# Optimization experiments

Hardware: AMD Instinct MI355X
Metric: run time of the kernel (lower is better)

## Reference

```python
import jax, jax.numpy as jnp
import numpy as np
import math

E, K, CAPF = 8, 2, 1.25
D, DFF = 512, 2048


def setup_inputs() -> dict:
    key = jax.random.key(0)
    ks = jax.random.split(key, 5)
    s = lambda k, sh, sc: (jax.random.normal(k, sh, jnp.float32) * sc)
    return {
        "x": jax.random.normal(ks[0], (8, 4096, D), jnp.float32),
        "Wr": s(ks[1], (D, E), 1.0 / math.sqrt(D)),
        "br": jnp.zeros((E,), jnp.float32),
        "W1": s(ks[2], (E, D, DFF), 1.0 / math.sqrt(D)),
        "b1": jnp.zeros((E, DFF), jnp.float32),
        "W2": s(ks[3], (E, DFF, D), 1.0 / math.sqrt(DFF)),
        "b2": jnp.zeros((E, D), jnp.float32),
    }


def _moe(x, Wr, br, W1, b1, W2, b2):
    orig = x.shape
    d = orig[-1]
    xf = x.reshape(-1, d)                     # [N, d]
    N = xf.shape[0]
    # --- TopK router ---
    logits = xf @ Wr + br                      # [N, E]
    probs = jax.nn.softmax(logits, axis=-1)
    topk_p, topk_i = jax.lax.top_k(probs, K)   # [N, K]
    topk_w = topk_p / (jnp.sum(topk_p, axis=-1, keepdims=True) + 1e-9)
    # --- Capacity-based sparse dispatch ---
    cap = max(1, int(math.ceil(CAPF * float(N * K) / float(E))))
    flat_e = topk_i.reshape(-1)                # [N*K] expert id per slot
    flat_w = topk_w.reshape(-1)                # [N*K]
    tok = jnp.repeat(jnp.arange(N), K)         # [N*K] source token id
    one_hot = jax.nn.one_hot(flat_e, E, dtype=xf.dtype)          # [N*K, E]
    pos = (jnp.cumsum(one_hot, axis=0) - one_hot)[jnp.arange(N * K), flat_e]
    pos = pos.astype(jnp.int32)                # position within expert buffer
    keep = pos < cap                           # tokens beyond capacity dropped
    w_k = jnp.where(keep, flat_w, 0.0)
    sum_w = jnp.zeros((N,), xf.dtype).at[tok].add(w_k)           # kept weight per token
    w_norm = w_k / (sum_w[tok] + 1e-9)
    slot = flat_e * cap + pos                  # flat index into [E*cap]
    slot_safe = jnp.where(keep, slot, E * cap) # out-of-bounds -> dropped by scatter
    expert_in = (jnp.zeros((E * cap, d), xf.dtype)
                 .at[slot_safe].set(xf[tok], mode="drop")
                 .reshape(E, cap, d))
    # --- Grouped expert FFN (exact GELU like torch nn.GELU) ---
    h = jax.nn.gelu(jnp.einsum("ecd,edf->ecf", expert_in, W1) + b1[:, None, :],
                    approximate=False)
    expert_out = (jnp.einsum("ecf,efd->ecd", h, W2) + b2[:, None, :]).reshape(E * cap, d)
    # --- Combine: gather back and weighted scatter-add per token ---
    contrib = expert_out[jnp.where(keep, slot, 0)]               # dropped -> w_norm=0
    y = jnp.zeros((N, d), xf.dtype).at[tok].add(contrib * w_norm[:, None])
    return y.reshape(orig)


def reference(x, Wr, br, W1, b1, W2, b2):
    return _moe(x, Wr, br, W1, b1, W2, b2)
```

## Files before the change

kernel.cpp:

```cpp
#include <hip/hip_runtime.h>
#include <cstdint>
#include <cstddef>

#define E_EXP 8
#define TOPK 2
#define DMODEL 512
#define DFFDIM 2048

typedef __attribute__((ext_vector_type(8))) short short8;
typedef __attribute__((ext_vector_type(4))) float f32x4;

__device__ __forceinline__ unsigned short f2bf(float f) {
    unsigned int u = __float_as_uint(f);
    u += 0x7fffu + ((u >> 16) & 1u);
    return (unsigned short)(u >> 16);
}

__device__ __forceinline__ void gld_lds16(const unsigned short* g, unsigned short* l) {
    __builtin_amdgcn_global_load_lds(
        (const __attribute__((address_space(1))) void*)g,
        (__attribute__((address_space(3))) void*)l, 16, 0, 0);
}

__global__ __launch_bounds__(256) void transpose_kernel(
    const float* __restrict__ in, unsigned short* __restrict__ out, int R, int C)
{
    __shared__ float tile[32][33];
    const float* ie = in + (size_t)blockIdx.z * R * C;
    unsigned short* oe = out + (size_t)blockIdx.z * R * C;
    int x = blockIdx.x * 32 + threadIdx.x;
#pragma unroll
    for (int i = 0; i < 4; i++) {
        int ry = blockIdx.y * 32 + threadIdx.y + i * 8;
        tile[threadIdx.y + i * 8][threadIdx.x] = ie[(size_t)ry * C + x];
    }
    __syncthreads();
    int xo = blockIdx.y * 32 + threadIdx.x;
#pragma unroll
    for (int i = 0; i < 4; i++) {
        int co = blockIdx.x * 32 + threadIdx.y + i * 8;
        oe[(size_t)co * R + xo] = f2bf(tile[threadIdx.x][threadIdx.y + i * 8]);
    }
}

__global__ __launch_bounds__(256) void router_kernel(
    const float* __restrict__ x, const float* __restrict__ Wr,
    const float* __restrict__ br, int N,
    int* __restrict__ e0e1, float2* __restrict__ w01)
{
    int lane = threadIdx.x & 63, wave = threadIdx.x >> 6;
    int t = blockIdx.x * 4 + wave;
    if (t >= N) return;
    const float* xr = x + (size_t)t * DMODEL;
    float4 v0 = *(const float4*)(xr + lane * 4);
    float4 v1 = *(const float4*)(xr + 256 + lane * 4);
    float xv[8] = {v0.x, v0.y, v0.z, v0.w, v1.x, v1.y, v1.z, v1.w};
    const float* wr0 = Wr + (size_t)lane * 32;
    const float* wr1 = Wr + (size_t)(256 + lane * 4) * 8;
    double acc[8];
#pragma unroll
    for (int j = 0; j < 8; j++) acc[j] = 0.0;
#pragma unroll
    for (int c = 0; c < 4; c++) {
#pragma unroll
        for (int j = 0; j < 8; j++) {
            acc[j] += (double)xv[c] * (double)wr0[c * 8 + j];
            acc[j] += (double)xv[4 + c] * (double)wr1[c * 8 + j];
        }
    }
#pragma unroll
    for (int j = 0; j < 8; j++) {
        double s = acc[j];
#pragma unroll
        for (int o = 32; o > 0; o >>= 1) s += __shfl_xor(s, o, 64);
        acc[j] = s;
    }
    if (lane == 0) {
        float l[8], p[8];
        float mx = -1e30f;
        for (int j = 0; j < 8; j++) { l[j] = (float)acc[j] + br[j]; mx = fmaxf(mx, l[j]); }
        float Z = 0.f;
        for (int j = 0; j < 8; j++) { p[j] = expf(l[j] - mx); Z += p[j]; }
        for (int j = 0; j < 8; j++) p[j] /= Z;
        int e0 = 0;
        for (int j = 1; j < 8; j++) if (l[j] > l[e0]) e0 = j;
        int e1 = (e0 == 0) ? 1 : 0;
        for (int j = 0; j < 8; j++) if (j != e0 && l[j] > l[e1]) e1 = j;
        float den = p[e0] + p[e1] + 1e-9f;
        e0e1[t] = e0 | (e1 << 8);
        w01[t] = make_float2(p[e0] / den, p[e1] / den);
    }
}

__global__ __launch_bounds__(256) void hist_kernel(
    const int* __restrict__ e0e1, int NK, int* __restrict__ hist)
{
    __shared__ int cnt[8];
    int t = threadIdx.x;
    if (t < 8) cnt[t] = 0;
    __syncthreads();
    int s = blockIdx.x * 256 + t;
    if (s < NK) {
        int pk = e0e1[s >> 1];
        int e = (s & 1) ? ((pk >> 8) & 255) : (pk & 255);
        atomicAdd(&cnt[e], 1);
    }
    __syncthreads();
    if (t < 8) hist[blockIdx.x * 8 + t] = cnt[t];
}

__global__ __launch_bounds__(256) void scan_kernel(
    const int* __restrict__ hist, int NB, int cap,
    int* __restrict__ base, int* __restrict__ cnt_used)
{
    __shared__ int buf[256];
    int t = threadIdx.x;
    for (int e = 0; e < 8; e++) {
        int v = (t < NB) ? hist[t * 8 + e] : 0;
        int val = v;
        buf[t] = val;
        __syncthreads();
        for (int o = 1; o < 256; o <<= 1) {
            int add = (t >= o) ? buf[t - o] : 0;
            __syncthreads();
            val += add;
            buf[t] = val;
            __syncthreads();
        }
        if (t < NB) base[t * 8 + e] = val - v;
        if (t == 255) cnt_used[e] = min(val, cap);
        __syncthreads();
    }
}

__global__ __launch_bounds__(256) void pos_kernel(
    const int* __restrict__ e0e1, const float2* __restrict__ w01,
    const int* __restrict__ base, int NK, int cap,
    int* __restrict__ sidx, int* __restrict__ tok_of, float* __restrict__ wslot)
{
    __shared__ int waveCnt[4][8];
    __shared__ float kw[256];
    int t = threadIdx.x, lane = t & 63, wave = t >> 6;
    int s = blockIdx.x * 256 + t;
    bool valid = s < NK;
    int e = 8; float w = 0.f;
    if (valid) {
        int pk = e0e1[s >> 1];
        float2 ww = w01[s >> 1];
        if (s & 1) { e = (pk >> 8) & 255; w = ww.y; }
        else       { e = pk & 255;        w = ww.x; }
    }
    unsigned long long mymask = 0ull;
#pragma unroll
    for (int j = 0; j < 8; j++) {
        unsigned long long m = __ballot(e == j);
        if (lane == j) waveCnt[wave][j] = __popcll(m);
        if (e == j) mymask = m;
    }
    __syncthreads();
    int wrank = __popcll(mymask & ((1ull << lane) - 1ull));
    int prior = 0;
    for (int w2 = 0; w2 < wave; w2++) prior += waveCnt[w2][e & 7];
    int pos = base[blockIdx.x * 8 + (e & 7)] + prior + wrank;
    bool keep = valid && (pos < cap);
    kw[t] = keep ? w : 0.f;
    __syncthreads();
    float sum = kw[t] + kw[t ^ 1];
    float wn = keep ? (kw[t] / (sum + 1e-9f)) : 0.f;
    if (valid) {
        int si = keep ? (e * cap + pos) : -1;
        sidx[s] = si;
        if (keep) { tok_of[si] = s >> 1; wslot[si] = wn; }
    }
}

__global__ __launch_bounds__(256) void scatter_kernel(
    const float* __restrict__ x, const int* __restrict__ sidx,
    unsigned short* __restrict__ Xe, int NK)
{
    int lane = threadIdx.x & 63, wave = threadIdx.x >> 6;
    int s = blockIdx.x * 4 + wave;
    if (s >= NK) return;
    int si = sidx[s];
    if (si < 0) return;
    int tok = s >> 1;
    const float* xr = x + (size_t)tok * DMODEL + lane * 8;
    float4 a = *(const float4*)xr;
    float4 b = *(const float4*)(xr + 4);
    short8 v;
    v[0] = (short)f2bf(a.x); v[1] = (short)f2bf(a.y);
    v[2] = (short)f2bf(a.z); v[3] = (short)f2bf(a.w);
    v[4] = (short)f2bf(b.x); v[5] = (short)f2bf(b.y);
    v[6] = (short)f2bf(b.z); v[7] = (short)f2bf(b.w);
    *(short8*)(Xe + (size_t)si * DMODEL + lane * 8) = v;
}

template <int MODE>
__global__ __launch_bounds__(256, 3) void gemm_kernel(
    const unsigned short* __restrict__ A, int lda, size_t aStrE,
    const unsigned short* __restrict__ B, int ldb, size_t bStrE,
    const float* __restrict__ bias, int biasStrE,
    void* __restrict__ out, size_t cStrE, int ldc,
    const int* __restrict__ cnt, const int* __restrict__ tok_of,
    const float* __restrict__ wslot, int cap, int Kext)
{
    __shared__ unsigned short As[2 * 128 * 32];
    __shared__ unsigned short Bs[2 * 128 * 32];
    int e = blockIdx.z;
    int m0 = blockIdx.y * 128, n0 = blockIdx.x * 128;
    int M = cnt[e];
    if (m0 >= M) return;
    const unsigned short* Ae = A + (size_t)e * aStrE;
    const unsigned short* Be = B + (size_t)e * bStrE;

    int t = threadIdx.x, lane = t & 63, wave = t >> 6;
    int row = t >> 2;
    int seg = ((t & 3) ^ ((t >> 3) & 3)) * 8;
    const unsigned short* ga = Ae + (size_t)(m0 + row) * lda + seg;
    const unsigned short* gb = Be + (size_t)(n0 + row) * ldb + seg;
    int wofs = __builtin_amdgcn_readfirstlane(wave * 512);

    f32x4 acc[4][4];
#pragma unroll
    for (int i = 0; i < 4; i++)
#pragma unroll
        for (int j = 0; j < 4; j++) acc[i][j] = (f32x4){0.f, 0.f, 0.f, 0.f};

    int wm = (wave & 1) * 64, wn = (wave >> 1) * 64;
    int lr = lane & 15, lq = lane >> 4;
    int sq = (lq ^ ((lr >> 1) & 3)) * 8;
    const unsigned short* pa = As + (wm + lr) * 32 + sq;
    const unsigned short* pb = Bs + (wn + lr) * 32 + sq;

    gld_lds16(ga, As + wofs);
    gld_lds16(ga + (size_t)64 * lda, As + 2048 + wofs);
    gld_lds16(gb, Bs + wofs);
    gld_lds16(gb + (size_t)64 * ldb, Bs + 2048 + wofs);
    ga += 32; gb += 32;
    __syncthreads();

    int buf = 0;
    for (int k0 = 32; k0 < Kext; k0 += 32) {
        int nbo = (buf ^ 1) * 4096;
        gld_lds16(ga, As + nbo + wofs);
        gld_lds16(ga + (size_t)64 * lda, As + nbo + 2048 + wofs);
        gld_lds16(gb, Bs + nbo + wofs);
        gld_lds16(gb + (size_t)64 * ldb, Bs + nbo + 2048 + wofs);
        ga += 32; gb += 32;
        {
            int bo = buf * 4096;
            short8 af[4], bfv[4];
#pragma unroll
            for (int i = 0; i < 4; i++) af[i] = *(const short8*)(pa + bo + i * 512);
#pragma unroll
            for (int j = 0; j < 4; j++) bfv[j] = *(const short8*)(pb + bo + j * 512);
#pragma unroll
            for (int i = 0; i < 4; i++)
#pragma unroll
                for (int j = 0; j < 4; j++)
                    acc[i][j] = __builtin_amdgcn_mfma_f32_16x16x32_bf16(af[i], bfv[j], acc[i][j], 0, 0, 0);
        }
        __syncthreads();
        buf ^= 1;
    }
    {
        int bo = buf * 4096;
        short8 af[4], bfv[4];
#pragma unroll
        for (int i = 0; i < 4; i++) af[i] = *(const short8*)(pa + bo + i * 512);
#pragma unroll
        for (int j = 0; j < 4; j++) bfv[j] = *(const short8*)(pb + bo + j * 512);
#pragma unroll
        for (int i = 0; i < 4; i++)
#pragma unroll
            for (int j = 0; j < 4; j++)
                acc[i][j] = __builtin_amdgcn_mfma_f32_16x16x32_bf16(af[i], bfv[j], acc[i][j], 0, 0, 0);
    }

    if (MODE == 0) {
        size_t cb = (size_t)e * cStrE;
#pragma unroll
        for (int j = 0; j < 4; j++) {
            int n = n0 + wn + j * 16 + lr;
            float bv = bias[(size_t)e * biasStrE + n];
#pragma unroll
            for (int i = 0; i < 4; i++) {
                int mbase = m0 + wm + i * 16 + lq * 4;
                f32x4 v = acc[i][j];
#pragma unroll
                for (int r = 0; r < 4; r++) {
                    float val = v[r] + bv;
                    val = 0.5f * val * (1.0f + erff(val * 0.7071067811865475f));
                    ((unsigned short*)out)[cb + (size_t)(mbase + r) * ldc + n] = f2bf(val);
                }
            }
        }
    } else {
        float wv[4][4]; int tv[4][4];
#pragma unroll
        for (int i = 0; i < 4; i++) {
            int mbase = m0 + wm + i * 16 + lq * 4;
#pragma unroll
            for (int r = 0; r < 4; r++) {
                int m = mbase + r;
                if (m < M) { int sl = e * cap + m; wv[i][r] = wslot[sl]; tv[i][r] = tok_of[sl]; }
                else       { wv[i][r] = 0.f; tv[i][r] = -1; }
            }
        }
        float* y = (float*)out;
#pragma unroll
        for (int j = 0; j < 4; j++) {
            int n = n0 + wn + j * 16 + lr;
            float bv = bias[(size_t)e * biasStrE + n];
#pragma unroll
            for (int i = 0; i < 4; i++) {
                f32x4 v = acc[i][j];
#pragma unroll
                for (int r = 0; r < 4; r++) {
                    if (tv[i][r] >= 0)
                        atomicAdd(y + (size_t)tv[i][r] * ldc + n, wv[i][r] * (v[r] + bv));
                }
            }
        }
    }
}

extern "C" void kernel_launch(void* const* d_in, const int* in_sizes, int n_in,
                              void* d_out, int out_size, void* d_ws, size_t ws_size,
                              hipStream_t stream)
{
    const float* x  = (const float*)d_in[0];
    const float* Wr = (const float*)d_in[1];
    const float* br = (const float*)d_in[2];
    const float* W1 = (const float*)d_in[3];
    const float* b1 = (const float*)d_in[4];
    const float* W2 = (const float*)d_in[5];
    const float* b2 = (const float*)d_in[6];
    float* y = (float*)d_out;
    (void)n_in;

    const int N = in_sizes[0] / DMODEL;
    const int NK = N * TOPK;
    const int cap = (NK * 5 + 31) / 32;
    const int mTiles = (cap + 127) / 128;
    const int NB = (NK + 255) / 256;

    size_t fixed = (size_t)E_EXP * DMODEL * DFFDIM * 2 * 2
                 + (size_t)E_EXP * cap * DMODEL * 2
                 + (size_t)N * 12 + (size_t)NK * 4 + (size_t)E_EXP * cap * 8
                 + (size_t)NB * 64 + (1 << 16);
    int G = E_EXP;
    while (G > 1 && fixed + (size_t)G * cap * DFFDIM * 2 > ws_size) G >>= 1;
    const int nGroups = E_EXP / G;

    char* ws = (char*)d_ws;
    size_t off = 0;
    auto take = [&](size_t bytes) {
        char* p = ws + off;
        off = (off + bytes + 255) & ~(size_t)255;
        return p;
    };
    unsigned short* W1t = (unsigned short*)take((size_t)E_EXP * DMODEL * DFFDIM * 2);
    unsigned short* W2t = (unsigned short*)take((size_t)E_EXP * DMODEL * DFFDIM * 2);
    unsigned short* Xe  = (unsigned short*)take((size_t)E_EXP * cap * DMODEL * 2);
    unsigned short* Hg  = (unsigned short*)take((size_t)G * cap * DFFDIM * 2);
    int*    e0e1 = (int*)take((size_t)N * 4);
    float2* w01  = (float2*)take((size_t)N * 8);
    int*    hist = (int*)take((size_t)NB * 8 * 4);
    int*    base = (int*)take((size_t)NB * 8 * 4);
    int*    cnt  = (int*)take(64);
    int*    sidx = (int*)take((size_t)NK * 4);
    int*    tok_of = (int*)take((size_t)E_EXP * cap * 4);
    float*  wslot  = (float*)take((size_t)E_EXP * cap * 4);

    transpose_kernel<<<dim3(DFFDIM / 32, DMODEL / 32, E_EXP), dim3(32, 8), 0, stream>>>(W1, W1t, DMODEL, DFFDIM);
    transpose_kernel<<<dim3(DMODEL / 32, DFFDIM / 32, E_EXP), dim3(32, 8), 0, stream>>>(W2, W2t, DFFDIM, DMODEL);
    router_kernel<<<(N + 3) / 4, 256, 0, stream>>>(x, Wr, br, N, e0e1, w01);
    hist_kernel<<<NB, 256, 0, stream>>>(e0e1, NK, hist);
    scan_kernel<<<1, 256, 0, stream>>>(hist, NB, cap, base, cnt);
    pos_kernel<<<NB, 256, 0, stream>>>(e0e1, w01, base, NK, cap, sidx, tok_of, wslot);
    scatter_kernel<<<(NK + 3) / 4, 256, 0, stream>>>(x, sidx, Xe, NK);
    hipMemsetAsync(d_out, 0, (size_t)out_size * 4, stream);

    for (int g = 0; g < nGroups; g++) {
        int e0 = g * G;
        gemm_kernel<0><<<dim3(DFFDIM / 128, mTiles, G), 256, 0, stream>>>(
            Xe + (size_t)e0 * cap * DMODEL, DMODEL, (size_t)cap * DMODEL,
            W1t + (size_t)e0 * DFFDIM * DMODEL, DMODEL, (size_t)DFFDIM * DMODEL,
            b1 + (size_t)e0 * DFFDIM, DFFDIM,
            Hg, (size_t)cap * DFFDIM, DFFDIM,
            cnt + e0, tok_of, wslot, cap, DMODEL);
        gemm_kernel<1><<<dim3(DMODEL / 128, mTiles, G), 256, 0, stream>>>(
            Hg, DFFDIM, (size_t)cap * DFFDIM,
            W2t + (size_t)e0 * DMODEL * DFFDIM, DFFDIM, (size_t)DMODEL * DFFDIM,
            b2 + (size_t)e0 * DMODEL, DMODEL,
            y, 0, DMODEL,
            cnt + e0, tok_of + (size_t)e0 * cap, wslot + (size_t)e0 * cap, cap, DFFDIM);
    }
}
```

Measured before the change: 993.6 us.

## Use 256x256 GEMM tiles and split DFF into four quarter passes

The expert GEMMs move from 128x128 tiles with 256 threads to 256x256 tiles with 512 threads, K-step 64, and a wider LDS swizzle. Larger tiles give more reuse per loaded byte. The FFN hidden dimension is now processed in four quarter-DFF passes over all experts. Each pass writes a smaller H buffer, and the second GEMM accumulates partial sums into y with atomics, adding bias only on the first pass. This trades a fixed, smaller workspace for four times as many atomic output updates and fewer blocks per launch, which risks tail and occupancy losses.

```diff
diff --git a/kernel.cpp b/kernel.cpp
--- a/kernel.cpp
+++ b/kernel.cpp
@@ -196,82 +196,104 @@
 }
 
 template <int MODE>
-__global__ __launch_bounds__(256, 3) void gemm_kernel(
+__global__ __launch_bounds__(512, 2) void gemm256_kernel(
     const unsigned short* __restrict__ A, int lda, size_t aStrE,
     const unsigned short* __restrict__ B, int ldb, size_t bStrE,
     const float* __restrict__ bias, int biasStrE,
     void* __restrict__ out, size_t cStrE, int ldc,
     const int* __restrict__ cnt, const int* __restrict__ tok_of,
-    const float* __restrict__ wslot, int cap, int Kext)
-{
-    __shared__ unsigned short As[2 * 128 * 32];
-    __shared__ unsigned short Bs[2 * 128 * 32];
+    const float* __restrict__ wslot, int cap, int Kext, int addBias)
+{
+    __shared__ unsigned short As[2 * 16384];
+    __shared__ unsigned short Bs[2 * 16384];
     int e = blockIdx.z;
-    int m0 = blockIdx.y * 128, n0 = blockIdx.x * 128;
+    int m0 = blockIdx.y * 256, n0 = blockIdx.x * 256;
     int M = cnt[e];
     if (m0 >= M) return;
     const unsigned short* Ae = A + (size_t)e * aStrE;
     const unsigned short* Be = B + (size_t)e * bStrE;
 
     int t = threadIdx.x, lane = t & 63, wave = t >> 6;
-    int row = t >> 2;
-    int seg = ((t & 3) ^ ((t >> 3) & 3)) * 8;
-    const unsigned short* ga = Ae + (size_t)(m0 + row) * lda + seg;
-    const unsigned short* gb = Be + (size_t)(n0 + row) * ldb + seg;
+    int srow = t >> 3;
+    int gseg = ((t & 7) ^ (srow & 7)) * 8;
+    const unsigned short* ga = Ae + (size_t)(m0 + srow) * lda + gseg;
+    const unsigned short* gb = Be + (size_t)(n0 + srow) * ldb + gseg;
     int wofs = __builtin_amdgcn_readfirstlane(wave * 512);
 
-    f32x4 acc[4][4];
-#pragma unroll
-    for (int i = 0; i < 4; i++)
+    f32x4 acc[8][4];
+#pragma unroll
+    for (int i = 0; i < 8; i++)
 #pragma unroll
         for (int j = 0; j < 4; j++) acc[i][j] = (f32x4){0.f, 0.f, 0.f, 0.f};
 
-    int wm = (wave & 1) * 64, wn = (wave >> 1) * 64;
+    int wm = (wave >> 2) * 128, wn = (wave & 3) * 64;
     int lr = lane & 15, lq = lane >> 4;
-    int sq = (lq ^ ((lr >> 1) & 3)) * 8;
-    const unsigned short* pa = As + (wm + lr) * 32 + sq;
-    const unsigned short* pb = Bs + (wn + lr) * 32 + sq;
-
-    gld_lds16(ga, As + wofs);
-    gld_lds16(ga + (size_t)64 * lda, As + 2048 + wofs);
-    gld_lds16(gb, Bs + wofs);
-    gld_lds16(gb + (size_t)64 * ldb, Bs + 2048 + wofs);
-    ga += 32; gb += 32;
+    int s0 = ((lq) ^ (lr & 7)) * 8;
+    int s1 = ((lq + 4) ^ (lr & 7)) * 8;
+    const unsigned short* pa = As + (wm + lr) * 64;
+    const unsigned short* pb = Bs + (wn + lr) * 64;
+
+    const int nt = Kext >> 6;
+
+#pragma unroll
+    for (int u = 0; u < 4; u++) {
+        gld_lds16(ga + (size_t)(u * 64) * lda, As + u * 4096 + wofs);
+        gld_lds16(gb + (size_t)(u * 64) * ldb, Bs + u * 4096 + wofs);
+    }
     __syncthreads();
 
     int buf = 0;
-    for (int k0 = 32; k0 < Kext; k0 += 32) {
-        int nbo = (buf ^ 1) * 4096;
-        gld_lds16(ga, As + nbo + wofs);
-        gld_lds16(ga + (size_t)64 * lda, As + nbo + 2048 + wofs);
-        gld_lds16(gb, Bs + nbo + wofs);
-        gld_lds16(gb + (size_t)64 * ldb, Bs + nbo + 2048 + wofs);
-        ga += 32; gb += 32;
+    for (int ks = 1; ks < nt; ks++) {
+        int nbo = (buf ^ 1) * 16384;
+        int k0 = ks * 64;
+#pragma unroll
+        for (int u = 0; u < 4; u++) {
+            gld_lds16(ga + (size_t)(u * 64) * lda + k0, As + nbo + u * 4096 + wofs);
+            gld_lds16(gb + (size_t)(u * 64) * ldb + k0, Bs + nbo + u * 4096 + wofs);
+        }
         {
-            int bo = buf * 4096;
-            short8 af[4], bfv[4];
-#pragma unroll
-            for (int i = 0; i < 4; i++) af[i] = *(const short8*)(pa + bo + i * 512);
-#pragma unroll
-            for (int j = 0; j < 4; j++) bfv[j] = *(const short8*)(pb + bo + j * 512);
-#pragma unroll
-            for (int i = 0; i < 4; i++)
+            int bo = buf * 16384;
+            short8 af[8], bfv[4];
+#pragma unroll
+            for (int i = 0; i < 8; i++) af[i] = *(const short8*)(pa + bo + i * 1024 + s0);
+#pragma unroll
+            for (int j = 0; j < 4; j++) bfv[j] = *(const short8*)(pb + bo + j * 1024 + s0);
+#pragma unroll
+            for (int i = 0; i < 8; i++)
 #pragma unroll
                 for (int j = 0; j < 4; j++)
                     acc[i][j] = __builtin_amdgcn_mfma_f32_16x16x32_bf16(af[i], bfv[j], acc[i][j], 0, 0, 0);
+#pragma unroll
+            for (int i = 0; i < 8; i++) af[i] = *(const short8*)(pa + bo + i * 1024 + s1);
+#pragma unroll
+            for (int j = 0; j < 4; j++) bfv[j] = *(const short8*)(pb + bo + j * 1024 + s1);
+#pragma unroll
+            for (int i = 0; i < 8; i++)
+#pragma unroll
+                for (int j = 0; j < 4; j++)
+                    acc[i][j] = __builtin_amdgcn_mfma_f32_16x16x32_bf16(af[i], bfv[j], acc[i][j], 0, 0, 0);
         }
         __syncthreads();
         buf ^= 1;
     }
     {
-        int bo = buf * 4096;
-        short8 af[4], bfv[4];
-#pragma unroll
-        for (int i = 0; i < 4; i++) af[i] = *(const short8*)(pa + bo + i * 512);
-#pragma unroll
-        for (int j = 0; j < 4; j++) bfv[j] = *(const short8*)(pb + bo + j * 512);
-#pragma unroll
-        for (int i = 0; i < 4; i++)
+        int bo = buf * 16384;
+        short8 af[8], bfv[4];
+#pragma unroll
+        for (int i = 0; i < 8; i++) af[i] = *(const short8*)(pa + bo + i * 1024 + s0);
+#pragma unroll
+        for (int j = 0; j < 4; j++) bfv[j] = *(const short8*)(pb + bo + j * 1024 + s0);
+#pragma unroll
+        for (int i = 0; i < 8; i++)
+#pragma unroll
+            for (int j = 0; j < 4; j++)
+                acc[i][j] = __builtin_amdgcn_mfma_f32_16x16x32_bf16(af[i], bfv[j], acc[i][j], 0, 0, 0);
+#pragma unroll
+        for (int i = 0; i < 8; i++) af[i] = *(const short8*)(pa + bo + i * 1024 + s1);
+#pragma unroll
+        for (int j = 0; j < 4; j++) bfv[j] = *(const short8*)(pb + bo + j * 1024 + s1);
+#pragma unroll
+        for (int i = 0; i < 8; i++)
 #pragma unroll
             for (int j = 0; j < 4; j++)
                 acc[i][j] = __builtin_amdgcn_mfma_f32_16x16x32_bf16(af[i], bfv[j], acc[i][j], 0, 0, 0);
@@ -284,7 +306,7 @@
             int n = n0 + wn + j * 16 + lr;
             float bv = bias[(size_t)e * biasStrE + n];
 #pragma unroll
-            for (int i = 0; i < 4; i++) {
+            for (int i = 0; i < 8; i++) {
                 int mbase = m0 + wm + i * 16 + lq * 4;
                 f32x4 v = acc[i][j];
 #pragma unroll
@@ -296,9 +318,9 @@
             }
         }
     } else {
-        float wv[4][4]; int tv[4][4];
-#pragma unroll
-        for (int i = 0; i < 4; i++) {
+        float wv[8][4]; int tv[8][4];
+#pragma unroll
+        for (int i = 0; i < 8; i++) {
             int mbase = m0 + wm + i * 16 + lq * 4;
 #pragma unroll
             for (int r = 0; r < 4; r++) {
@@ -311,9 +333,9 @@
 #pragma unroll
         for (int j = 0; j < 4; j++) {
             int n = n0 + wn + j * 16 + lr;
-            float bv = bias[(size_t)e * biasStrE + n];
-#pragma unroll
-            for (int i = 0; i < 4; i++) {
+            float bv = addBias ? bias[(size_t)e * biasStrE + n] : 0.f;
+#pragma unroll
+            for (int i = 0; i < 8; i++) {
                 f32x4 v = acc[i][j];
 #pragma unroll
                 for (int r = 0; r < 4; r++) {
@@ -337,21 +359,14 @@
     const float* W2 = (const float*)d_in[5];
     const float* b2 = (const float*)d_in[6];
     float* y = (float*)d_out;
-    (void)n_in;
+    (void)n_in; (void)ws_size;
 
     const int N = in_sizes[0] / DMODEL;
     const int NK = N * TOPK;
     const int cap = (NK * 5 + 31) / 32;
-    const int mTiles = (cap + 127) / 128;
+    const int mT = (cap + 255) / 256;
     const int NB = (NK + 255) / 256;
-
-    size_t fixed = (size_t)E_EXP * DMODEL * DFFDIM * 2 * 2
-                 + (size_t)E_EXP * cap * DMODEL * 2
-                 + (size_t)N * 12 + (size_t)NK * 4 + (size_t)E_EXP * cap * 8
-                 + (size_t)NB * 64 + (1 << 16);
-    int G = E_EXP;
-    while (G > 1 && fixed + (size_t)G * cap * DFFDIM * 2 > ws_size) G >>= 1;
-    const int nGroups = E_EXP / G;
+    const int QD = DFFDIM / 4;
 
     char* ws = (char*)d_ws;
     size_t off = 0;
@@ -363,7 +378,7 @@
     unsigned short* W1t = (unsigned short*)take((size_t)E_EXP * DMODEL * DFFDIM * 2);
     unsigned short* W2t = (unsigned short*)take((size_t)E_EXP * DMODEL * DFFDIM * 2);
     unsigned short* Xe  = (unsigned short*)take((size_t)E_EXP * cap * DMODEL * 2);
-    unsigned short* Hg  = (unsigned short*)take((size_t)G * cap * DFFDIM * 2);
+    unsigned short* Hg  = (unsigned short*)take((size_t)E_EXP * cap * QD * 2);
     int*    e0e1 = (int*)take((size_t)N * 4);
     float2* w01  = (float2*)take((size_t)N * 8);
     int*    hist = (int*)take((size_t)NB * 8 * 4);
@@ -382,19 +397,18 @@
     scatter_kernel<<<(NK + 3) / 4, 256, 0, stream>>>(x, sidx, Xe, NK);
     hipMemsetAsync(d_out, 0, (size_t)out_size * 4, stream);
 
-    for (int g = 0; g < nGroups; g++) {
-        int e0 = g * G;
-        gemm_kernel<0><<<dim3(DFFDIM / 128, mTiles, G), 256, 0, stream>>>(
-            Xe + (size_t)e0 * cap * DMODEL, DMODEL, (size_t)cap * DMODEL,
-            W1t + (size_t)e0 * DFFDIM * DMODEL, DMODEL, (size_t)DFFDIM * DMODEL,
-            b1 + (size_t)e0 * DFFDIM, DFFDIM,
-            Hg, (size_t)cap * DFFDIM, DFFDIM,
-            cnt + e0, tok_of, wslot, cap, DMODEL);
-        gemm_kernel<1><<<dim3(DMODEL / 128, mTiles, G), 256, 0, stream>>>(
-            Hg, DFFDIM, (size_t)cap * DFFDIM,
-            W2t + (size_t)e0 * DMODEL * DFFDIM, DFFDIM, (size_t)DMODEL * DFFDIM,
-            b2 + (size_t)e0 * DMODEL, DMODEL,
+    for (int q = 0; q < 4; q++) {
+        gemm256_kernel<0><<<dim3(QD / 256, mT, E_EXP), 512, 0, stream>>>(
+            Xe, DMODEL, (size_t)cap * DMODEL,
+            W1t + (size_t)q * QD * DMODEL, DMODEL, (size_t)DFFDIM * DMODEL,
+            b1 + q * QD, DFFDIM,
+            Hg, (size_t)cap * QD, QD,
+            cnt, tok_of, wslot, cap, DMODEL, 1);
+        gemm256_kernel<1><<<dim3(DMODEL / 256, mT, E_EXP), 512, 0, stream>>>(
+            Hg, QD, (size_t)cap * QD,
+            W2t + (size_t)q * QD, DFFDIM, (size_t)DMODEL * DFFDIM,
+            b2, DMODEL,
             y, 0, DMODEL,
-            cnt + e0, tok_of + (size_t)e0 * cap, wslot + (size_t)e0 * cap, cap, DFFDIM);
-    }
-}
+            cnt, tok_of, wslot, cap, QD, q == 0 ? 1 : 0);
+    }
+}
```

Measured after the change: 1.468 ms. +47.8%, slower.

## Fuse expert FFN GEMMs with gather into one persistent per-tile kernel

Applied to the files above, without the earlier changes.

Replaces the scatter kernel and the two grouped GEMM launches with a single kernel. Each block gathers its 128 routed token rows straight from x, converting them to bf16 in registers. It then streams W1 and W2 in 32-column DFF chunks, applies GELU on chip and accumulates the output projection in registers before the atomic combine. This removes the bf16 Xe buffer and the large H intermediate round trip through memory, along with several launches. In exchange, each block rereads its expert's full weights. Register pressure is high (a 128-float accumulator per lane plus the cached A fragments), and the tile count assumes cap is a multiple of 128.

```diff
diff --git a/kernel.cpp b/kernel.cpp
--- a/kernel.cpp
+++ b/kernel.cpp
@@ -136,7 +136,7 @@
 __global__ __launch_bounds__(256) void pos_kernel(
     const int* __restrict__ e0e1, const float2* __restrict__ w01,
     const int* __restrict__ base, int NK, int cap,
-    int* __restrict__ sidx, int* __restrict__ tok_of, float* __restrict__ wslot)
+    int* __restrict__ tok_of, float* __restrict__ wslot)
 {
     __shared__ int waveCnt[4][8];
     __shared__ float kw[256];
@@ -167,160 +167,142 @@
     __syncthreads();
     float sum = kw[t] + kw[t ^ 1];
     float wn = keep ? (kw[t] / (sum + 1e-9f)) : 0.f;
-    if (valid) {
-        int si = keep ? (e * cap + pos) : -1;
-        sidx[s] = si;
-        if (keep) { tok_of[si] = s >> 1; wslot[si] = wn; }
-    }
-}
-
-__global__ __launch_bounds__(256) void scatter_kernel(
-    const float* __restrict__ x, const int* __restrict__ sidx,
-    unsigned short* __restrict__ Xe, int NK)
-{
-    int lane = threadIdx.x & 63, wave = threadIdx.x >> 6;
-    int s = blockIdx.x * 4 + wave;
-    if (s >= NK) return;
-    int si = sidx[s];
-    if (si < 0) return;
-    int tok = s >> 1;
-    const float* xr = x + (size_t)tok * DMODEL + lane * 8;
-    float4 a = *(const float4*)xr;
-    float4 b = *(const float4*)(xr + 4);
-    short8 v;
-    v[0] = (short)f2bf(a.x); v[1] = (short)f2bf(a.y);
-    v[2] = (short)f2bf(a.z); v[3] = (short)f2bf(a.w);
-    v[4] = (short)f2bf(b.x); v[5] = (short)f2bf(b.y);
-    v[6] = (short)f2bf(b.z); v[7] = (short)f2bf(b.w);
-    *(short8*)(Xe + (size_t)si * DMODEL + lane * 8) = v;
-}
-
-template <int MODE>
-__global__ __launch_bounds__(256, 3) void gemm_kernel(
-    const unsigned short* __restrict__ A, int lda, size_t aStrE,
-    const unsigned short* __restrict__ B, int ldb, size_t bStrE,
-    const float* __restrict__ bias, int biasStrE,
-    void* __restrict__ out, size_t cStrE, int ldc,
+    if (keep) {
+        int si = e * cap + pos;
+        tok_of[si] = s >> 1;
+        wslot[si] = wn;
+    }
+}
+
+__global__ __launch_bounds__(512, 2) void fused_ffn_kernel(
+    const float* __restrict__ x,
+    const unsigned short* __restrict__ W1t,
+    const float* __restrict__ b1,
+    const unsigned short* __restrict__ W2t,
+    const float* __restrict__ b2,
+    float* __restrict__ y,
     const int* __restrict__ cnt, const int* __restrict__ tok_of,
-    const float* __restrict__ wslot, int cap, int Kext)
-{
-    __shared__ unsigned short As[2 * 128 * 32];
-    __shared__ unsigned short Bs[2 * 128 * 32];
-    int e = blockIdx.z;
-    int m0 = blockIdx.y * 128, n0 = blockIdx.x * 128;
+    const float* __restrict__ wslot, int cap)
+{
+    __shared__ unsigned short Wb[2][32768];
+    __shared__ unsigned short Hlds[8 * 640];
+
+    int b = blockIdx.x;
+    int e = b & 7, mtile = b >> 3;
+    int m0 = mtile * 128;
     int M = cnt[e];
     if (m0 >= M) return;
-    const unsigned short* Ae = A + (size_t)e * aStrE;
-    const unsigned short* Be = B + (size_t)e * bStrE;
-
-    int t = threadIdx.x, lane = t & 63, wave = t >> 6;
-    int row = t >> 2;
-    int seg = ((t & 3) ^ ((t >> 3) & 3)) * 8;
-    const unsigned short* ga = Ae + (size_t)(m0 + row) * lda + seg;
-    const unsigned short* gb = Be + (size_t)(n0 + row) * ldb + seg;
-    int wofs = __builtin_amdgcn_readfirstlane(wave * 512);
-
-    f32x4 acc[4][4];
-#pragma unroll
-    for (int i = 0; i < 4; i++)
-#pragma unroll
-        for (int j = 0; j < 4; j++) acc[i][j] = (f32x4){0.f, 0.f, 0.f, 0.f};
-
-    int wm = (wave & 1) * 64, wn = (wave >> 1) * 64;
+
+    int t = threadIdx.x, lane = t & 63, w = t >> 6;
     int lr = lane & 15, lq = lane >> 4;
-    int sq = (lq ^ ((lr >> 1) & 3)) * 8;
-    const unsigned short* pa = As + (wm + lr) * 32 + sq;
-    const unsigned short* pb = Bs + (wn + lr) * 32 + sq;
-
-    gld_lds16(ga, As + wofs);
-    gld_lds16(ga + (size_t)64 * lda, As + 2048 + wofs);
-    gld_lds16(gb, Bs + wofs);
-    gld_lds16(gb + (size_t)64 * ldb, Bs + 2048 + wofs);
-    ga += 32; gb += 32;
+
+    const unsigned short* W1e = W1t + (size_t)e * DFFDIM * DMODEL;
+    const unsigned short* W2e = W2t + (size_t)e * DMODEL * DFFDIM;
+
+    int mrowA = m0 + w * 16 + lr;
+    int tokA = (mrowA < M) ? tok_of[e * cap + mrowA] : -1;
+    const float* xr = x + (size_t)(tokA < 0 ? 0 : tokA) * DMODEL;
+    short8 a_frag[16];
+#pragma unroll
+    for (int kf = 0; kf < 16; kf++) {
+        float4 u0 = *(const float4*)(xr + kf * 32 + lq * 8);
+        float4 u1 = *(const float4*)(xr + kf * 32 + lq * 8 + 4);
+        short8 f;
+        f[0] = (short)f2bf(u0.x); f[1] = (short)f2bf(u0.y);
+        f[2] = (short)f2bf(u0.z); f[3] = (short)f2bf(u0.w);
+        f[4] = (short)f2bf(u1.x); f[5] = (short)f2bf(u1.y);
+        f[6] = (short)f2bf(u1.z); f[7] = (short)f2bf(u1.w);
+        if (tokA < 0) f = (short8){0, 0, 0, 0, 0, 0, 0, 0};
+        a_frag[kf] = f;
+    }
+
+    f32x4 yac[32];
+#pragma unroll
+    for (int j = 0; j < 32; j++) yac[j] = (f32x4){0.f, 0.f, 0.f, 0.f};
+
+    unsigned short* Hl = Hlds + w * 640;
+    int l2 = lane >> 2;
+    int w2seg = (((lane & 3) ^ (l2 & 3)) * 8);
+    int w1seg = (lane ^ w) * 8;
+
+    {
+        int f0 = 0;
+#pragma unroll
+        for (int q = 0; q < 4; q++) {
+            int f = q * 8 + w;
+            gld_lds16(W1e + (size_t)(f0 + f) * DMODEL + w1seg,
+                      &Wb[0][q * 4096 + w * 512]);
+            int n = q * 128 + w * 16 + l2;
+            gld_lds16(W2e + (size_t)n * DFFDIM + f0 + w2seg,
+                      &Wb[0][16384 + q * 4096 + w * 512]);
+        }
+    }
     __syncthreads();
 
     int buf = 0;
-    for (int k0 = 32; k0 < Kext; k0 += 32) {
-        int nbo = (buf ^ 1) * 4096;
-        gld_lds16(ga, As + nbo + wofs);
-        gld_lds16(ga + (size_t)64 * lda, As + nbo + 2048 + wofs);
-        gld_lds16(gb, Bs + nbo + wofs);
-        gld_lds16(gb + (size_t)64 * ldb, Bs + nbo + 2048 + wofs);
-        ga += 32; gb += 32;
-        {
-            int bo = buf * 4096;
-            short8 af[4], bfv[4];
-#pragma unroll
-            for (int i = 0; i < 4; i++) af[i] = *(const short8*)(pa + bo + i * 512);
-#pragma unroll
-            for (int j = 0; j < 4; j++) bfv[j] = *(const short8*)(pb + bo + j * 512);
-#pragma unroll
-            for (int i = 0; i < 4; i++)
-#pragma unroll
-                for (int j = 0; j < 4; j++)
-                    acc[i][j] = __builtin_amdgcn_mfma_f32_16x16x32_bf16(af[i], bfv[j], acc[i][j], 0, 0, 0);
+    for (int c = 0; c < 64; c++) {
+        if (c < 63) {
+            int f0 = (c + 1) * 32;
+#pragma unroll
+            for (int q = 0; q < 4; q++) {
+                int f = q * 8 + w;
+                gld_lds16(W1e + (size_t)(f0 + f) * DMODEL + w1seg,
+                          &Wb[buf ^ 1][q * 4096 + w * 512]);
+                int n = q * 128 + w * 16 + l2;
+                gld_lds16(W2e + (size_t)n * DFFDIM + f0 + w2seg,
+                          &Wb[buf ^ 1][16384 + q * 4096 + w * 512]);
+            }
+        }
+        const unsigned short* W1b = &Wb[buf][0];
+        const unsigned short* W2b = &Wb[buf][16384];
+        f32x4 h0 = (f32x4){0.f, 0.f, 0.f, 0.f};
+        f32x4 h1 = (f32x4){0.f, 0.f, 0.f, 0.f};
+#pragma unroll
+        for (int kf = 0; kf < 16; kf++) {
+            int s6 = ((kf * 4 + lq) ^ (lr & 7)) * 8;
+            short8 bf0 = *(const short8*)(W1b + lr * 512 + s6);
+            short8 bf1 = *(const short8*)(W1b + (16 + lr) * 512 + s6);
+            h0 = __builtin_amdgcn_mfma_f32_16x16x32_bf16(a_frag[kf], bf0, h0, 0, 0, 0);
+            h1 = __builtin_amdgcn_mfma_f32_16x16x32_bf16(a_frag[kf], bf1, h1, 0, 0, 0);
+        }
+        int f0 = c * 32;
+        float b1v0 = b1[e * DFFDIM + f0 + lr];
+        float b1v1 = b1[e * DFFDIM + f0 + 16 + lr];
+#pragma unroll
+        for (int r = 0; r < 4; r++) {
+            float v0 = h0[r] + b1v0;
+            v0 = 0.5f * v0 * (1.0f + erff(v0 * 0.7071067811865475f));
+            float v1 = h1[r] + b1v1;
+            v1 = 0.5f * v1 * (1.0f + erff(v1 * 0.7071067811865475f));
+            Hl[(lq * 4 + r) * 40 + lr] = f2bf(v0);
+            Hl[(lq * 4 + r) * 40 + 16 + lr] = f2bf(v1);
+        }
+        short8 a2 = *(const short8*)(Hl + lr * 40 + lq * 8);
+#pragma unroll
+        for (int j = 0; j < 32; j++) {
+            short8 b2f = *(const short8*)(W2b + (16 * j + lr) * 32 + ((lq ^ (lr & 3)) * 8));
+            yac[j] = __builtin_amdgcn_mfma_f32_16x16x32_bf16(a2, b2f, yac[j], 0, 0, 0);
         }
         __syncthreads();
         buf ^= 1;
     }
-    {
-        int bo = buf * 4096;
-        short8 af[4], bfv[4];
-#pragma unroll
-        for (int i = 0; i < 4; i++) af[i] = *(const short8*)(pa + bo + i * 512);
-#pragma unroll
-        for (int j = 0; j < 4; j++) bfv[j] = *(const short8*)(pb + bo + j * 512);
-#pragma unroll
-        for (int i = 0; i < 4; i++)
-#pragma unroll
-            for (int j = 0; j < 4; j++)
-                acc[i][j] = __builtin_amdgcn_mfma_f32_16x16x32_bf16(af[i], bfv[j], acc[i][j], 0, 0, 0);
-    }
-
-    if (MODE == 0) {
-        size_t cb = (size_t)e * cStrE;
-#pragma unroll
-        for (int j = 0; j < 4; j++) {
-            int n = n0 + wn + j * 16 + lr;
-            float bv = bias[(size_t)e * biasStrE + n];
-#pragma unroll
-            for (int i = 0; i < 4; i++) {
-                int mbase = m0 + wm + i * 16 + lq * 4;
-                f32x4 v = acc[i][j];
-#pragma unroll
-                for (int r = 0; r < 4; r++) {
-                    float val = v[r] + bv;
-                    val = 0.5f * val * (1.0f + erff(val * 0.7071067811865475f));
-                    ((unsigned short*)out)[cb + (size_t)(mbase + r) * ldc + n] = f2bf(val);
-                }
-            }
-        }
-    } else {
-        float wv[4][4]; int tv[4][4];
-#pragma unroll
-        for (int i = 0; i < 4; i++) {
-            int mbase = m0 + wm + i * 16 + lq * 4;
-#pragma unroll
-            for (int r = 0; r < 4; r++) {
-                int m = mbase + r;
-                if (m < M) { int sl = e * cap + m; wv[i][r] = wslot[sl]; tv[i][r] = tok_of[sl]; }
-                else       { wv[i][r] = 0.f; tv[i][r] = -1; }
-            }
-        }
-        float* y = (float*)out;
-#pragma unroll
-        for (int j = 0; j < 4; j++) {
-            int n = n0 + wn + j * 16 + lr;
-            float bv = bias[(size_t)e * biasStrE + n];
-#pragma unroll
-            for (int i = 0; i < 4; i++) {
-                f32x4 v = acc[i][j];
-#pragma unroll
-                for (int r = 0; r < 4; r++) {
-                    if (tv[i][r] >= 0)
-                        atomicAdd(y + (size_t)tv[i][r] * ldc + n, wv[i][r] * (v[r] + bv));
-                }
-            }
+
+    int tokC[4]; float wC[4];
+#pragma unroll
+    for (int r = 0; r < 4; r++) {
+        int m = m0 + w * 16 + lq * 4 + r;
+        if (m < M) { tokC[r] = tok_of[e * cap + m]; wC[r] = wslot[e * cap + m]; }
+        else       { tokC[r] = -1; wC[r] = 0.f; }
+    }
+#pragma unroll
+    for (int j = 0; j < 32; j++) {
+        int n = 16 * j + lr;
+        float b2v = b2[e * DMODEL + n];
+        f32x4 v = yac[j];
+#pragma unroll
+        for (int r = 0; r < 4; r++) {
+            if (tokC[r] >= 0)
+                atomicAdd(y + (size_t)tokC[r] * DMODEL + n, wC[r] * (v[r] + b2v));
         }
     }
 }
@@ -337,21 +319,13 @@
     const float* W2 = (const float*)d_in[5];
     const float* b2 = (const float*)d_in[6];
     float* y = (float*)d_out;
-    (void)n_in;
+    (void)n_in; (void)ws_size;
 
     const int N = in_sizes[0] / DMODEL;
     const int NK = N * TOPK;
     const int cap = (NK * 5 + 31) / 32;
-    const int mTiles = (cap + 127) / 128;
     const int NB = (NK + 255) / 256;
-
-    size_t fixed = (size_t)E_EXP * DMODEL * DFFDIM * 2 * 2
-                 + (size_t)E_EXP * cap * DMODEL * 2
-                 + (size_t)N * 12 + (size_t)NK * 4 + (size_t)E_EXP * cap * 8
-                 + (size_t)NB * 64 + (1 << 16);
-    int G = E_EXP;
-    while (G > 1 && fixed + (size_t)G * cap * DFFDIM * 2 > ws_size) G >>= 1;
-    const int nGroups = E_EXP / G;
+    const int mT = cap / 128;
 
     char* ws = (char*)d_ws;
     size_t off = 0;
@@ -362,14 +336,11 @@
     };
     unsigned short* W1t = (unsigned short*)take((size_t)E_EXP * DMODEL * DFFDIM * 2);
     unsigned short* W2t = (unsigned short*)take((size_t)E_EXP * DMODEL * DFFDIM * 2);
-    unsigned short* Xe  = (unsigned short*)take((size_t)E_EXP * cap * DMODEL * 2);
-    unsigned short* Hg  = (unsigned short*)take((size_t)G * cap * DFFDIM * 2);
     int*    e0e1 = (int*)take((size_t)N * 4);
     float2* w01  = (float2*)take((size_t)N * 8);
     int*    hist = (int*)take((size_t)NB * 8 * 4);
     int*    base = (int*)take((size_t)NB * 8 * 4);
     int*    cnt  = (int*)take(64);
-    int*    sidx = (int*)take((size_t)NK * 4);
     int*    tok_of = (int*)take((size_t)E_EXP * cap * 4);
     float*  wslot  = (float*)take((size_t)E_EXP * cap * 4);
 
@@ -378,23 +349,9 @@
     router_kernel<<<(N + 3) / 4, 256, 0, stream>>>(x, Wr, br, N, e0e1, w01);
     hist_kernel<<<NB, 256, 0, stream>>>(e0e1, NK, hist);
     scan_kernel<<<1, 256, 0, stream>>>(hist, NB, cap, base, cnt);
-    pos_kernel<<<NB, 256, 0, stream>>>(e0e1, w01, base, NK, cap, sidx, tok_of, wslot);
-    scatter_kernel<<<(NK + 3) / 4, 256, 0, stream>>>(x, sidx, Xe, NK);
+    pos_kernel<<<NB, 256, 0, stream>>>(e0e1, w01, base, NK, cap, tok_of, wslot);
     hipMemsetAsync(d_out, 0, (size_t)out_size * 4, stream);
 
-    for (int g = 0; g < nGroups; g++) {
-        int e0 = g * G;
-        gemm_kernel<0><<<dim3(DFFDIM / 128, mTiles, G), 256, 0, stream>>>(
-            Xe + (size_t)e0 * cap * DMODEL, DMODEL, (size_t)cap * DMODEL,
-            W1t + (size_t)e0 * DFFDIM * DMODEL, DMODEL, (size_t)DFFDIM * DMODEL,
-            b1 + (size_t)e0 * DFFDIM, DFFDIM,
-            Hg, (size_t)cap * DFFDIM, DFFDIM,
-            cnt + e0, tok_of, wslot, cap, DMODEL);
-        gemm_kernel<1><<<dim3(DMODEL / 128, mTiles, G), 256, 0, stream>>>(
-            Hg, DFFDIM, (size_t)cap * DFFDIM,
-            W2t + (size_t)e0 * DMODEL * DFFDIM, DFFDIM, (size_t)DMODEL * DFFDIM,
-            b2 + (size_t)e0 * DMODEL, DMODEL,
-            y, 0, DMODEL,
-            cnt + e0, tok_of + (size_t)e0 * cap, wslot + (size_t)e0 * cap, cap, DFFDIM);
-    }
-}
+    fused_ffn_kernel<<<E_EXP * mT, 512, 0, stream>>>(
+        x, W1t, b1, W2t, b2, y, cnt, tok_of, wslot, cap);
+}
```

Result: slower. 1.075 ms (+8.2%).
